# Performance work log

Hardware: AMD Instinct MI355X
Metric: run time of the kernel (lower is better)

## Reference

```python
import jax, jax.numpy as jnp
import numpy as np

B, T, C, H = 4, 2048, 1024, 16
D = C // H  # head_dim = 64


def setup_inputs() -> dict:
    key = jax.random.key(0)
    ks = jax.random.split(key, 5)
    s = 0.02
    return {
        "x": jax.random.normal(ks[0], (B, T, C), dtype=jnp.float32),
        "w_qkv": jax.random.normal(ks[1], (C, 3 * C), dtype=jnp.float32) * s,
        "b_qkv": jnp.zeros((3 * C,), dtype=jnp.float32),
        "w_proj": jax.random.normal(ks[2], (C, C), dtype=jnp.float32) * s,
        "b_proj": jnp.zeros((C,), dtype=jnp.float32),
    }


def reference(x, w_qkv, b_qkv, w_proj, b_proj):
    Bx, Tx, Cx = x.shape
    qkv = x @ w_qkv + b_qkv                      # [B,T,3C]
    q, k, v = jnp.split(qkv, 3, axis=-1)
    # [B,T,C] -> [B,H,T,D]
    q = q.reshape(Bx, Tx, H, D).transpose(0, 2, 1, 3)
    k = k.reshape(Bx, Tx, H, D).transpose(0, 2, 1, 3)
    v = v.reshape(Bx, Tx, H, D).transpose(0, 2, 1, 3)
    scale = 1.0 / np.sqrt(D).astype(np.float32)
    attn = jnp.einsum('bhqd,bhkd->bhqk', q, k) * scale   # [B,H,T,T]
    causal = jnp.tril(jnp.ones((Tx, Tx), dtype=bool))
    attn = jnp.where(causal[None, None], attn, -jnp.inf)
    attn = jax.nn.softmax(attn, axis=-1)
    out = jnp.einsum('bhqk,bhkd->bhqd', attn, v)          # [B,H,T,D]
    out = out.transpose(0, 2, 1, 3).reshape(Bx, Tx, Cx)   # [B,T,C]
    return out @ w_proj + b_proj
```

## Files before the change

kernel.cpp:

```cpp
#include <hip/hip_runtime.h>
#include <hip/hip_bf16.h>
#include <math.h>

using bf16 = __hip_bfloat16;
typedef __bf16 bf16x8 __attribute__((ext_vector_type(8)));
typedef float  f32x4  __attribute__((ext_vector_type(4)));
typedef unsigned short ushort8 __attribute__((ext_vector_type(8)));
typedef unsigned uint4v __attribute__((ext_vector_type(4)));

#define DEV __device__ __forceinline__

DEV void gld_lds16(const void* g, void* l) {
    __builtin_amdgcn_global_load_lds((const __attribute__((address_space(1))) void*)g,
                                     (__attribute__((address_space(3))) void*)l,
                                     16, 0, 0);
}

__global__ __launch_bounds__(256) void prep(const float* __restrict__ x,
                                            bf16* __restrict__ xb,
                                            const float* __restrict__ w_qkv,
                                            bf16* __restrict__ wqkvT,
                                            const float* __restrict__ w_proj,
                                            bf16* __restrict__ wprojT) {
    __shared__ float tile[32][33];
    int blk = blockIdx.x;
    int tid = threadIdx.x;
    if (blk < 8192) {
        int i = blk * 256 + tid;
        float4 f = ((const float4*)x)[i];
        __align__(8) bf16 o[4] = {__float2bfloat16(f.x), __float2bfloat16(f.y),
                                  __float2bfloat16(f.z), __float2bfloat16(f.w)};
        ((uint64_t*)xb)[i] = *(const uint64_t*)o;
        return;
    }
    const float* in;
    bf16* out;
    int R, Cn, bx, by;
    if (blk < 11264) {
        int bid = blk - 8192;
        in = w_qkv; out = wqkvT; R = 1024; Cn = 3072;
        bx = (bid % 96) * 32; by = (bid / 96) * 32;
    } else {
        int bid = blk - 11264;
        in = w_proj; out = wprojT; R = 1024; Cn = 1024;
        bx = (bid % 32) * 32; by = (bid / 32) * 32;
    }
    int tx = tid & 31, ty = tid >> 5;
    for (int i = ty; i < 32; i += 8)
        tile[i][tx] = in[(size_t)(by + i) * Cn + bx + tx];
    __syncthreads();
    for (int i = ty; i < 32; i += 8)
        out[(size_t)(bx + i) * R + by + tx] = __float2bfloat16(tile[tx][i]);
}

__global__ __launch_bounds__(256) void gemm_qkv(const bf16* __restrict__ A,
                                                const bf16* __restrict__ Bt,
                                                const float* __restrict__ bias,
                                                bf16* __restrict__ qb,
                                                bf16* __restrict__ kb,
                                                bf16* __restrict__ vTb) {
    constexpr int K = 1024, T = 2048;
    constexpr float CS = 0.18033688f;
    __shared__ __align__(16) bf16 Al[128 * 32];
    __shared__ __align__(16) bf16 Bl[128 * 32];
    __shared__ __align__(16) bf16 Et[32 * 136];
    int tid = threadIdx.x;
    int lane = tid & 63, w = tid >> 6;
    int wm = w >> 1, wn = w & 1;
    int l15 = lane & 15, quad = lane >> 4;
    int m0 = blockIdx.x * 128, n0 = blockIdx.y * 128;
    int l3 = l15 & 3;

    f32x4 acc[4][4] = {};
    for (int k0 = 0; k0 < K; k0 += 32) {
        __syncthreads();
        for (int it = 0; it < 2; ++it) {
            int e = (it * 256 + tid) * 8;
            int r = e >> 5, cu = (e >> 3) & 3;
            int cs = ((cu ^ (r & 3)) << 3);
            gld_lds16(A  + (size_t)(m0 + r) * K + k0 + cs, &Al[e]);
            gld_lds16(Bt + (size_t)(n0 + r) * K + k0 + cs, &Bl[e]);
        }
        __syncthreads();
        bf16x8 af[4], bfr[4];
        for (int i = 0; i < 4; ++i)
            af[i] = *(const bf16x8*)&Al[(wm * 64 + i * 16 + l15) * 32 + ((quad ^ l3) << 3)];
        for (int j = 0; j < 4; ++j)
            bfr[j] = *(const bf16x8*)&Bl[(wn * 64 + j * 16 + l15) * 32 + ((quad ^ l3) << 3)];
        for (int i = 0; i < 4; ++i)
            for (int j = 0; j < 4; ++j)
                acc[i][j] = __builtin_amdgcn_mfma_f32_16x16x32_bf16(af[i], bfr[j], acc[i][j], 0, 0, 0);
    }

    int mode = (blockIdx.y < 8) ? 0 : (blockIdx.y < 16 ? 1 : 2);
    float bv[4];
    for (int j = 0; j < 4; ++j)
        bv[j] = bias[n0 + wn * 64 + j * 16 + l15];
    float scl = (mode == 0) ? CS : 1.0f;

    for (int i = 0; i < 4; ++i) {
        __syncthreads();
        for (int j = 0; j < 4; ++j)
            for (int v = 0; v < 4; ++v)
                Et[(wm * 16 + quad * 4 + v) * 136 + wn * 64 + j * 16 + l15] =
                    __float2bfloat16((acc[i][j][v] + bv[j]) * scl);
        __syncthreads();
        if (mode < 2) {
            int r = tid >> 3, cc = (tid & 7) * 16;
            int m = m0 + i * 16 + (r < 16 ? r : r + 48);
            int b = m >> 11, t = m & 2047;
            int n = (n0 & 1023) + cc;
            int h = n >> 6, d = n & 63;
            bf16* dst = (mode == 0 ? qb : kb) + (((size_t)(b * 16 + h)) * T + t) * 64 + d;
            ushort8 u0 = *(const ushort8*)&Et[r * 136 + cc];
            ushort8 u1 = *(const ushort8*)&Et[r * 136 + cc + 8];
            *(ushort8*)dst = u0;
            *(ushort8*)(dst + 8) = u1;
        } else {
            int run = tid >> 7, d = tid & 127;
            int t0 = m0 + i * 16 + run * 64;
            int b = t0 >> 11, tt = t0 & 2047;
            int n = (n0 & 1023) + d;
            int h = n >> 6, dd = n & 63;
            __align__(16) bf16 tmp[16];
            for (int jj = 0; jj < 16; ++jj)
                tmp[jj] = Et[(run * 16 + jj) * 136 + d];
            bf16* dst = vTb + (((size_t)(b * 16 + h)) * 64 + dd) * T + tt;
            *(ushort8*)dst = *(const ushort8*)tmp;
            *(ushort8*)(dst + 8) = *(const ushort8*)(tmp + 8);
        }
    }
}

__global__ __launch_bounds__(256, 4) void flash_attn(const bf16* __restrict__ qb,
                                                     const bf16* __restrict__ kbuf,
                                                     const bf16* __restrict__ vT,
                                                     bf16* __restrict__ ob) {
    constexpr int T = 2048;
    __shared__ __align__(16) bf16 Kl[2][64 * 64];
    __shared__ __align__(16) bf16 Vl[2][64 * 64];
    int tid = threadIdx.x;
    int lane = tid & 63, w = tid >> 6;
    int l15 = lane & 15, quad = lane >> 4;

    int g = blockIdx.x;
    int quarter = g >> 8;
    int j = (g >> 6) & 3;
    int bh = g & 63;
    int xq;
    switch (quarter) {
        case 0:  xq = 15 - j; break;
        case 1:  xq = 8 + j;  break;
        case 2:  xq = 4 + j;  break;
        default: xq = 3 - j;  break;
    }
    int q0 = xq << 7;
    const bf16* qbase = qb   + (size_t)bh * T * 64;
    const bf16* kbase = kbuf + (size_t)bh * T * 64;
    const bf16* vbase = vT   + (size_t)bh * 64 * T;

    int qg[2];
    bf16x8 qa[2][2];
#pragma unroll
    for (int s = 0; s < 2; ++s) {
        qg[s] = q0 + w * 32 + s * 16 + l15;
#pragma unroll
        for (int c = 0; c < 2; ++c)
            qa[s][c] = *(const bf16x8*)(qbase + (size_t)qg[s] * 64 + c * 32 + quad * 8);
    }

    bf16x8 ones;
#pragma unroll
    for (int i = 0; i < 8; ++i) ones[i] = (__bf16)1.0f;

    f32x4 O[2][4] = {};
    f32x4 O1[2] = {};
    int h7 = l15 & 7;

    int off0 = tid * 8, off1 = (256 + tid) * 8;
    int r0 = off0 >> 6, cb0 = (off0 >> 3) & 7;
    int r1 = off1 >> 6, cb1 = (off1 >> 3) & 7;
    int kc0 = (cb0 ^ (r0 & 7)) << 3, kc1 = (cb1 ^ (r1 & 7)) << 3;

    int nit = 2 * xq + 2;

    bf16x8 vr0 = *(const bf16x8*)(vbase + (size_t)r0 * T + kc0);
    bf16x8 vr1 = *(const bf16x8*)(vbase + (size_t)r1 * T + kc1);
    gld_lds16(kbase + (size_t)r0 * 64 + kc0, &Kl[0][off0]);
    gld_lds16(kbase + (size_t)r1 * 64 + kc1, &Kl[0][off1]);
    *(bf16x8*)&Vl[0][off0] = vr0;
    *(bf16x8*)&Vl[0][off1] = vr1;

    for (int t = 0; t < nit; ++t) {
        int cur = t & 1, nxt = cur ^ 1;
        __syncthreads();
        bool pre = (t + 1 < nit);
        if (pre) {
            int kb2 = (t + 1) << 6;
            vr0 = *(const bf16x8*)(vbase + (size_t)r0 * T + kb2 + kc0);
            vr1 = *(const bf16x8*)(vbase + (size_t)r1 * T + kb2 + kc1);
            gld_lds16(kbase + (size_t)(kb2 + r0) * 64 + kc0, &Kl[nxt][off0]);
            gld_lds16(kbase + (size_t)(kb2 + r1) * 64 + kc1, &Kl[nxt][off1]);
        }
        int kb = t << 6;
        bool maskt = (t >= nit - 2);

        unsigned Dq[2][4][2];
#pragma unroll
        for (int jn = 0; jn < 4; ++jn) {
            int row = jn * 16 + l15;
            bf16x8 a0 = *(const bf16x8*)&Kl[cur][row * 64 + ((quad ^ h7) << 3)];
            bf16x8 a1 = *(const bf16x8*)&Kl[cur][row * 64 + (((4 + quad) ^ h7) << 3)];
            f32x4 sa[2] = {};
            __builtin_amdgcn_s_setprio(1);
            sa[0] = __builtin_amdgcn_mfma_f32_16x16x32_bf16(a0, qa[0][0], sa[0], 0, 0, 0);
            sa[0] = __builtin_amdgcn_mfma_f32_16x16x32_bf16(a1, qa[0][1], sa[0], 0, 0, 0);
            sa[1] = __builtin_amdgcn_mfma_f32_16x16x32_bf16(a0, qa[1][0], sa[1], 0, 0, 0);
            sa[1] = __builtin_amdgcn_mfma_f32_16x16x32_bf16(a1, qa[1][1], sa[1], 0, 0, 0);
            __builtin_amdgcn_s_setprio(0);
#pragma unroll
            for (int s = 0; s < 2; ++s) {
                float p[4];
#pragma unroll
                for (int v = 0; v < 4; ++v) {
                    float e = __builtin_amdgcn_exp2f(sa[s][v]);
                    if (maskt) {
                        int key = kb + jn * 16 + quad * 4 + v;
                        e = (key <= qg[s]) ? e : 0.f;
                    }
                    p[v] = e;
                }
                unsigned lo, hi;
                asm("v_cvt_pk_bf16_f32 %0, %1, %2" : "=v"(lo) : "v"(p[0]), "v"(p[1]));
                asm("v_cvt_pk_bf16_f32 %0, %1, %2" : "=v"(hi) : "v"(p[2]), "v"(p[3]));
                Dq[s][jn][0] = lo;
                Dq[s][jn][1] = hi;
            }
        }

        bf16x8 pf[2][2];
#pragma unroll
        for (int s = 0; s < 2; ++s)
#pragma unroll
            for (int c = 0; c < 2; ++c) {
                uint4v wv;
#pragma unroll
                for (int h = 0; h < 2; ++h) {
                    unsigned X = Dq[s][2 * c][h];
                    unsigned Y = Dq[s][2 * c + 1][h];
                    asm("v_permlane32_swap_b32 %0, %1" : "+v"(X), "+v"(Y));
                    asm("v_permlane16_swap_b32 %0, %1" : "+v"(X), "+v"(Y));
                    wv[h]     = X;
                    wv[2 + h] = Y;
                }
                pf[s][c] = __builtin_bit_cast(bf16x8, wv);
            }

        __builtin_amdgcn_s_setprio(1);
#pragma unroll
        for (int s = 0; s < 2; ++s) {
            O1[s] = __builtin_amdgcn_mfma_f32_16x16x32_bf16(pf[s][0], ones, O1[s], 0, 0, 0);
            O1[s] = __builtin_amdgcn_mfma_f32_16x16x32_bf16(pf[s][1], ones, O1[s], 0, 0, 0);
        }
        __builtin_amdgcn_s_setprio(0);

#pragma unroll
        for (int jd = 0; jd < 4; ++jd) {
            int vrow = jd * 16 + l15;
            bf16x8 v0 = *(const bf16x8*)&Vl[cur][vrow * 64 + ((quad ^ h7) << 3)];
            bf16x8 v1 = *(const bf16x8*)&Vl[cur][vrow * 64 + (((4 + quad) ^ h7) << 3)];
            __builtin_amdgcn_s_setprio(1);
            O[0][jd] = __builtin_amdgcn_mfma_f32_16x16x32_bf16(pf[0][0], v0, O[0][jd], 0, 0, 0);
            O[0][jd] = __builtin_amdgcn_mfma_f32_16x16x32_bf16(pf[0][1], v1, O[0][jd], 0, 0, 0);
            O[1][jd] = __builtin_amdgcn_mfma_f32_16x16x32_bf16(pf[1][0], v0, O[1][jd], 0, 0, 0);
            O[1][jd] = __builtin_amdgcn_mfma_f32_16x16x32_bf16(pf[1][1], v1, O[1][jd], 0, 0, 0);
            __builtin_amdgcn_s_setprio(0);
        }

        if (pre) {
            *(bf16x8*)&Vl[nxt][off0] = vr0;
            *(bf16x8*)&Vl[nxt][off1] = vr1;
        }
    }

    int b = bh >> 4, h = bh & 15;
#pragma unroll
    for (int s = 0; s < 2; ++s) {
        float linv[4];
#pragma unroll
        for (int v = 0; v < 4; ++v) linv[v] = 1.f / O1[s][v];
#pragma unroll
        for (int jd = 0; jd < 4; ++jd) {
#pragma unroll
            for (int v = 0; v < 4; ++v) {
                int qr = q0 + w * 32 + s * 16 + quad * 4 + v;
                ob[((size_t)(b * T + qr)) * 1024 + h * 64 + jd * 16 + l15] =
                    __float2bfloat16(O[s][jd][v] * linv[v]);
            }
        }
    }
}

__global__ __launch_bounds__(256) void gemm_proj(const bf16* __restrict__ A,
                                                 const bf16* __restrict__ Bt,
                                                 const float* __restrict__ bias,
                                                 float* __restrict__ out) {
    constexpr int K = 1024, N = 1024;
    __shared__ __align__(16) bf16 Al[128 * 32];
    __shared__ __align__(16) bf16 Bl[128 * 32];
    int tid = threadIdx.x;
    int lane = tid & 63, w = tid >> 6;
    int wm = w >> 1, wn = w & 1;
    int l15 = lane & 15, quad = lane >> 4;
    int m0 = blockIdx.x * 128, n0 = blockIdx.y * 128;
    int l3 = l15 & 3;

    f32x4 acc[4][4] = {};
    for (int k0 = 0; k0 < K; k0 += 32) {
        __syncthreads();
        for (int it = 0; it < 2; ++it) {
            int e = (it * 256 + tid) * 8;
            int r = e >> 5, cu = (e >> 3) & 3;
            int cs = ((cu ^ (r & 3)) << 3);
            gld_lds16(A  + (size_t)(m0 + r) * K + k0 + cs, &Al[e]);
            gld_lds16(Bt + (size_t)(n0 + r) * K + k0 + cs, &Bl[e]);
        }
        __syncthreads();
        bf16x8 af[4], bfr[4];
        for (int i = 0; i < 4; ++i)
            af[i] = *(const bf16x8*)&Al[(wm * 64 + i * 16 + l15) * 32 + ((quad ^ l3) << 3)];
        for (int j = 0; j < 4; ++j)
            bfr[j] = *(const bf16x8*)&Bl[(wn * 64 + j * 16 + l15) * 32 + ((quad ^ l3) << 3)];
        for (int i = 0; i < 4; ++i)
            for (int j = 0; j < 4; ++j)
                acc[i][j] = __builtin_amdgcn_mfma_f32_16x16x32_bf16(af[i], bfr[j], acc[i][j], 0, 0, 0);
    }
    for (int i = 0; i < 4; ++i) {
        int mbase = m0 + wm * 64 + i * 16 + quad * 4;
        for (int j = 0; j < 4; ++j) {
            int n = n0 + wn * 64 + j * 16 + l15;
            float bv = bias[n];
            for (int v = 0; v < 4; ++v)
                out[(size_t)(mbase + v) * N + n] = acc[i][j][v] + bv;
        }
    }
}

extern "C" void kernel_launch(void* const* d_in, const int* in_sizes, int n_in,
                              void* d_out, int out_size, void* d_ws, size_t ws_size,
                              hipStream_t stream) {
    (void)in_sizes; (void)n_in; (void)out_size; (void)ws_size;
    const float* x      = (const float*)d_in[0];
    const float* w_qkv  = (const float*)d_in[1];
    const float* b_qkv  = (const float*)d_in[2];
    const float* w_proj = (const float*)d_in[3];
    const float* b_proj = (const float*)d_in[4];
    float* out = (float*)d_out;

    char* ws = (char*)d_ws;
    bf16* xb     = (bf16*)(ws);
    bf16* wqkvT  = (bf16*)(ws + (16u << 20));
    bf16* wprojT = (bf16*)(ws + (22u << 20));
    bf16* qbuf   = (bf16*)(ws + (24u << 20));
    bf16* kbuf   = (bf16*)(ws + (40u << 20));
    bf16* vTb    = (bf16*)(ws + (72u << 20));
    bf16* ob     = (bf16*)(ws + (56u << 20));

    prep<<<12288, 256, 0, stream>>>(x, xb, w_qkv, wqkvT, w_proj, wprojT);
    gemm_qkv<<<dim3(64, 24), 256, 0, stream>>>(xb, wqkvT, b_qkv, qbuf, kbuf, vTb);
    flash_attn<<<1024, 256, 0, stream>>>(qbuf, kbuf, vTb, ob);
    gemm_proj<<<dim3(64, 8), 256, 0, stream>>>(ob, wprojT, b_proj, out);
}
```

Measured before the change: 238.4 us.

## Rewrite QKV GEMM as 256x256 tile with double-buffered 8-wave pipelined schedule

The QKV projection GEMM moves from 128x128 tiles with 4 waves and one sync per k-step to 256x256 tiles with 8 waves, 64-wide k-steps and a double-buffered LDS ping-pong. Global-to-LDS loads are interleaved with MFMA quadrants under explicit vmcnt waits, barriers and setprio. A swizzled 1D block index is added for L2 locality. This is meant to hide load latency and raise reuse, at the cost of 128KB of LDS, one block per CU and a more fragile hand-tuned schedule.

```diff
diff --git a/kernel.cpp b/kernel.cpp
--- a/kernel.cpp
+++ b/kernel.cpp
@@ -53,80 +53,125 @@
         out[(size_t)(bx + i) * R + by + tx] = __float2bfloat16(tile[tx][i]);
 }
 
-__global__ __launch_bounds__(256) void gemm_qkv(const bf16* __restrict__ A,
+__global__ __launch_bounds__(512) void gemm_qkv(const bf16* __restrict__ A,
                                                 const bf16* __restrict__ Bt,
                                                 const float* __restrict__ bias,
                                                 bf16* __restrict__ qb,
                                                 bf16* __restrict__ kb,
                                                 bf16* __restrict__ vTb) {
-    constexpr int K = 1024, T = 2048;
+    constexpr int K = 1024;
     constexpr float CS = 0.18033688f;
-    __shared__ __align__(16) bf16 Al[128 * 32];
-    __shared__ __align__(16) bf16 Bl[128 * 32];
-    __shared__ __align__(16) bf16 Et[32 * 136];
+    __shared__ __align__(16) bf16 SM[65536];
     int tid = threadIdx.x;
-    int lane = tid & 63, w = tid >> 6;
-    int wm = w >> 1, wn = w & 1;
+    int lane = tid & 63, wid = tid >> 6;
+    int wm = wid >> 2, wn = wid & 3;
     int l15 = lane & 15, quad = lane >> 4;
-    int m0 = blockIdx.x * 128, n0 = blockIdx.y * 128;
-    int l3 = l15 & 3;
-
-    f32x4 acc[4][4] = {};
-    for (int k0 = 0; k0 < K; k0 += 32) {
+    int h7 = l15 & 7;
+
+    int wg = blockIdx.x;
+    int swz = (wg & 7) * 48 + (wg >> 3);
+    int bx = swz & 31, by = swz >> 5;
+    int m0 = bx * 256, n0 = by * 256;
+
+    int r0s = tid >> 3;
+    int sc0 = (((tid & 7) ^ (r0s & 7)) << 3);
+    int bstr = tid >> 8;
+    int brow = (tid >> 3) & 31;
+
+    f32x4 acc[8][4] = {};
+    bf16x8 afr[4][2], bfr[2][2];
+
+#define STAGE_A(buf, mh, kt) do {                                                 \
+    gld_lds16(A + (size_t)(m0 + (mh)*64 + r0s) * K + (kt)*64 + sc0,               \
+              &SM[((buf)*2 + (mh)) * 8192 + tid * 8]);                            \
+    gld_lds16(A + (size_t)(m0 + 128 + (mh)*64 + r0s) * K + (kt)*64 + sc0,         \
+              &SM[((buf)*2 + (mh)) * 8192 + 4096 + tid * 8]); } while (0)
+#define STAGE_B(buf, nh, kt) do {                                                 \
+    gld_lds16(Bt + (size_t)(n0 + bstr*64 + (nh)*32 + brow) * K + (kt)*64 + sc0,   \
+              &SM[32768 + ((buf)*2 + (nh)) * 8192 + tid * 8]);                    \
+    gld_lds16(Bt + (size_t)(n0 + 128 + bstr*64 + (nh)*32 + brow) * K + (kt)*64 + sc0, \
+              &SM[32768 + ((buf)*2 + (nh)) * 8192 + 4096 + tid * 8]); } while (0)
+#define LOAD_A(buf, mh) do {                                                      \
+    const bf16* ab = &SM[((buf)*2 + (mh)) * 8192 + wm * 4096];                    \
+    for (int i = 0; i < 4; ++i)                                                   \
+        for (int kc = 0; kc < 2; ++kc)                                            \
+            afr[i][kc] = *(const bf16x8*)&ab[(i*16 + l15) * 64 +                  \
+                                             (((kc*4 + quad) ^ h7) << 3)]; } while (0)
+#define LOAD_B(buf, nh) do {                                                      \
+    const bf16* bb = &SM[32768 + ((buf)*2 + (nh)) * 8192 + wn * 2048];            \
+    for (int j = 0; j < 2; ++j)                                                   \
+        for (int kc = 0; kc < 2; ++kc)                                            \
+            bfr[j][kc] = *(const bf16x8*)&bb[(j*16 + l15) * 64 +                  \
+                                             (((kc*4 + quad) ^ h7) << 3)]; } while (0)
+#define MFMA_Q(mh, nh) do {                                                       \
+    __builtin_amdgcn_s_setprio(1);                                                \
+    for (int i = 0; i < 4; ++i)                                                   \
+        for (int j = 0; j < 2; ++j)                                               \
+            for (int kc = 0; kc < 2; ++kc)                                        \
+                acc[(mh)*4 + i][(nh)*2 + j] = __builtin_amdgcn_mfma_f32_16x16x32_bf16( \
+                    afr[i][kc], bfr[j][kc], acc[(mh)*4 + i][(nh)*2 + j], 0, 0, 0); \
+    __builtin_amdgcn_s_setprio(0); } while (0)
+#define VM6 asm volatile("s_waitcnt vmcnt(6)" ::: "memory")
+#define BARP do { __builtin_amdgcn_s_barrier(); __builtin_amdgcn_sched_barrier(0); } while (0)
+
+    STAGE_A(0, 0, 0); STAGE_B(0, 0, 0); STAGE_B(0, 1, 0); STAGE_A(0, 1, 0);
+
+#pragma unroll 1
+    for (int t = 0; t < 8; ++t) {
+        int ktA = 2 * t + 1, ktB = 2 * t + 2;
+        STAGE_A(1, 0, ktA); VM6; BARP; LOAD_A(0, 0); LOAD_B(0, 0); MFMA_Q(0, 0);
+        STAGE_B(1, 0, ktA); VM6; BARP; LOAD_B(0, 1);               MFMA_Q(0, 1);
+        STAGE_B(1, 1, ktA); VM6; BARP; LOAD_A(0, 1);               MFMA_Q(1, 1);
+        STAGE_A(1, 1, ktA);      BARP; LOAD_B(0, 0);               MFMA_Q(1, 0);
+        STAGE_A(0, 0, ktB); VM6; BARP; LOAD_A(1, 0); LOAD_B(1, 0); MFMA_Q(0, 0);
+        STAGE_B(0, 0, ktB); VM6; BARP; LOAD_B(1, 1);               MFMA_Q(0, 1);
+        STAGE_B(0, 1, ktB); VM6; BARP; LOAD_A(1, 1);               MFMA_Q(1, 1);
+        STAGE_A(0, 1, ktB);      BARP; LOAD_B(1, 0);               MFMA_Q(1, 0);
+    }
+#undef STAGE_A
+#undef STAGE_B
+#undef LOAD_A
+#undef LOAD_B
+#undef MFMA_Q
+#undef VM6
+#undef BARP
+
+    asm volatile("s_waitcnt vmcnt(0)" ::: "memory");
+
+    int mode = by >> 2;
+    float scl = (mode == 0) ? CS : 1.0f;
+    float bv[4];
+    for (int nj = 0; nj < 4; ++nj)
+        bv[nj] = bias[n0 + wn * 64 + nj * 16 + l15];
+    bf16* Et = &SM[0];
+
+    for (int ai = 0; ai < 8; ++ai) {
         __syncthreads();
-        for (int it = 0; it < 2; ++it) {
-            int e = (it * 256 + tid) * 8;
-            int r = e >> 5, cu = (e >> 3) & 3;
-            int cs = ((cu ^ (r & 3)) << 3);
-            gld_lds16(A  + (size_t)(m0 + r) * K + k0 + cs, &Al[e]);
-            gld_lds16(Bt + (size_t)(n0 + r) * K + k0 + cs, &Bl[e]);
-        }
-        __syncthreads();
-        bf16x8 af[4], bfr[4];
-        for (int i = 0; i < 4; ++i)
-            af[i] = *(const bf16x8*)&Al[(wm * 64 + i * 16 + l15) * 32 + ((quad ^ l3) << 3)];
-        for (int j = 0; j < 4; ++j)
-            bfr[j] = *(const bf16x8*)&Bl[(wn * 64 + j * 16 + l15) * 32 + ((quad ^ l3) << 3)];
-        for (int i = 0; i < 4; ++i)
-            for (int j = 0; j < 4; ++j)
-                acc[i][j] = __builtin_amdgcn_mfma_f32_16x16x32_bf16(af[i], bfr[j], acc[i][j], 0, 0, 0);
-    }
-
-    int mode = (blockIdx.y < 8) ? 0 : (blockIdx.y < 16 ? 1 : 2);
-    float bv[4];
-    for (int j = 0; j < 4; ++j)
-        bv[j] = bias[n0 + wn * 64 + j * 16 + l15];
-    float scl = (mode == 0) ? CS : 1.0f;
-
-    for (int i = 0; i < 4; ++i) {
-        __syncthreads();
-        for (int j = 0; j < 4; ++j)
+        for (int nj = 0; nj < 4; ++nj)
             for (int v = 0; v < 4; ++v)
-                Et[(wm * 16 + quad * 4 + v) * 136 + wn * 64 + j * 16 + l15] =
-                    __float2bfloat16((acc[i][j][v] + bv[j]) * scl);
+                Et[(wm * 16 + quad * 4 + v) * 264 + wn * 64 + nj * 16 + l15] =
+                    __float2bfloat16((acc[ai][nj][v] + bv[nj]) * scl);
         __syncthreads();
         if (mode < 2) {
-            int r = tid >> 3, cc = (tid & 7) * 16;
-            int m = m0 + i * 16 + (r < 16 ? r : r + 48);
+            int r = tid >> 4, ck = tid & 15;
+            int m = m0 + (r >> 4) * 128 + ai * 16 + (r & 15);
             int b = m >> 11, t = m & 2047;
-            int n = (n0 & 1023) + cc;
+            int n = (n0 & 1023) + ck * 16;
             int h = n >> 6, d = n & 63;
-            bf16* dst = (mode == 0 ? qb : kb) + (((size_t)(b * 16 + h)) * T + t) * 64 + d;
-            ushort8 u0 = *(const ushort8*)&Et[r * 136 + cc];
-            ushort8 u1 = *(const ushort8*)&Et[r * 136 + cc + 8];
-            *(ushort8*)dst = u0;
-            *(ushort8*)(dst + 8) = u1;
+            bf16* dst = (mode == 0 ? qb : kb) + (((size_t)(b * 16 + h)) * 2048 + t) * 64 + d;
+            *(ushort8*)dst       = *(const ushort8*)&Et[r * 264 + ck * 16];
+            *(ushort8*)(dst + 8) = *(const ushort8*)&Et[r * 264 + ck * 16 + 8];
         } else {
-            int run = tid >> 7, d = tid & 127;
-            int t0 = m0 + i * 16 + run * 64;
+            int tg = tid >> 8, d = tid & 255;
+            int t0 = m0 + tg * 128 + ai * 16;
             int b = t0 >> 11, tt = t0 & 2047;
             int n = (n0 & 1023) + d;
             int h = n >> 6, dd = n & 63;
             __align__(16) bf16 tmp[16];
             for (int jj = 0; jj < 16; ++jj)
-                tmp[jj] = Et[(run * 16 + jj) * 136 + d];
-            bf16* dst = vTb + (((size_t)(b * 16 + h)) * 64 + dd) * T + tt;
-            *(ushort8*)dst = *(const ushort8*)tmp;
+                tmp[jj] = Et[(tg * 16 + jj) * 264 + d];
+            bf16* dst = vTb + (((size_t)(b * 16 + h)) * 64 + dd) * 2048 + tt;
+            *(ushort8*)dst       = *(const ushort8*)tmp;
             *(ushort8*)(dst + 8) = *(const ushort8*)(tmp + 8);
         }
     }
@@ -367,7 +412,7 @@
     bf16* ob     = (bf16*)(ws + (56u << 20));
 
     prep<<<12288, 256, 0, stream>>>(x, xb, w_qkv, wqkvT, w_proj, wprojT);
-    gemm_qkv<<<dim3(64, 24), 256, 0, stream>>>(xb, wqkvT, b_qkv, qbuf, kbuf, vTb);
+    gemm_qkv<<<384, 512, 0, stream>>>(xb, wqkvT, b_qkv, qbuf, kbuf, vTb);
     flash_attn<<<1024, 256, 0, stream>>>(qbuf, kbuf, vTb, ob);
     gemm_proj<<<dim3(64, 8), 256, 0, stream>>>(ob, wprojT, b_proj, out);
 }
```

Result: slower. 247.7 us (+3.9%).
